# Kernel optimization log

Hardware: AMD Instinct MI355X
Metric: run time of the kernel (lower is better)

## Reference

```python
import jax, jax.numpy as jnp
import numpy as np


def _ln(x, g, b):
    m = x.mean(-1, keepdims=True)
    v = ((x - m) ** 2).mean(-1, keepdims=True)
    return (x - m) * jax.lax.rsqrt(v + 1e-5) * g + b


def _forward(x, fx_in, pre_w1, pre_b1, pre_w2, pre_b2, placeholder,
             ln1_g, ln1_b, px_w, px_b, pfx_w, pfx_b, slice_w, slice_b, temp,
             q_w, k_w, v_w, out_w, out_b, ln2_g, ln2_b,
             mlp_w1, mlp_b1, mlp_w2, mlp_b2,
             ln3_g, ln3_b, head_w1, head_b1, head_w2, head_b2):
    # All linear weights are stored as [in, out] (pre-transposed vs torch nn.Linear).
    B, N, _ = x.shape
    L, H = temp.shape
    dh = slice_w.shape[1]
    gelu = lambda t: jax.nn.gelu(t, approximate=False)
    # preprocess MLP (n_layers=0, res=False): Linear -> GELU -> Linear
    h = jnp.concatenate([x, fx_in], axis=-1)
    h = gelu(h @ pre_w1 + pre_b1) @ pre_w2 + pre_b2
    h = h + placeholder  # learned [D] offset
    scale = 1.0 / jnp.sqrt(jnp.asarray(dh, h.dtype))
    for i in range(L):  # loop over structurally distinct layers
        y = _ln(h, ln1_g[i], ln1_b[i])
        # project to per-head features: bhnd
        fx_mid = (y @ pfx_w[i] + pfx_b[i]).reshape(B, N, H, dh).transpose(0, 2, 1, 3)
        x_mid = (y @ px_w[i] + px_b[i]).reshape(B, N, H, dh).transpose(0, 2, 1, 3)
        # soft slice assignment over G slices
        logits = jnp.einsum('bhnd,dg->bhng', x_mid, slice_w[i]) + slice_b[i]
        sw = jax.nn.softmax(logits / temp[i][None, :, None, None], axis=-1)  # bhng
        norm = sw.sum(axis=2)  # bhg
        tok = jnp.einsum('bhnd,bhng->bhgd', fx_mid, sw) / (norm + 1e-5)[..., None]
        # attention over G=slice_num tokens
        q = tok @ q_w[i]
        k = tok @ k_w[i]
        v = tok @ v_w[i]
        attn = jax.nn.softmax(jnp.einsum('bhgd,bhmd->bhgm', q, k) * scale, axis=-1)
        out_slice = jnp.einsum('bhgm,bhmd->bhgd', attn, v)
        # deslice back to points
        out_x = jnp.einsum('bhgd,bhng->bhnd', out_slice, sw)
        out_x = out_x.transpose(0, 2, 1, 3).reshape(B, N, H * dh)
        h = h + (out_x @ out_w[i] + out_b[i])
        z = _ln(h, ln2_g[i], ln2_b[i])
        h = h + (gelu(z @ mlp_w1[i] + mlp_b1[i]) @ mlp_w2[i] + mlp_b2[i])
    z = _ln(h, ln3_g, ln3_b)
    return gelu(z @ head_w1 + head_b1) @ head_w2 + head_b2


def setup_inputs() -> dict:
    key = jax.random.key(0)
    B, N, D, H, dh, G, L = 2, 16384, 256, 8, 32, 64, 5
    SP, FUN, OUT = 2, 4, 4
    ID = H * dh  # inner_dim == n_hidden
    MR = D * 1   # mlp_ratio=1
    ks = iter(jax.random.split(key, 64))
    nrm = lambda shape, s=0.02: jax.random.normal(next(ks), shape, jnp.float32) * s
    return dict(
        x=jax.random.normal(next(ks), (B, N, SP), jnp.float32),
        fx_in=jax.random.normal(next(ks), (B, N, FUN), jnp.float32),
        pre_w1=nrm((SP + FUN, 2 * D)), pre_b1=jnp.zeros((2 * D,), jnp.float32),
        pre_w2=nrm((2 * D, D)), pre_b2=jnp.zeros((D,), jnp.float32),
        placeholder=nrm((D,)),
        ln1_g=jnp.ones((L, D), jnp.float32), ln1_b=jnp.zeros((L, D), jnp.float32),
        px_w=nrm((L, D, ID)), px_b=jnp.zeros((L, ID), jnp.float32),
        pfx_w=nrm((L, D, ID)), pfx_b=jnp.zeros((L, ID), jnp.float32),
        slice_w=nrm((L, dh, G), 0.1), slice_b=jnp.zeros((L, G), jnp.float32),
        temp=0.5 * jnp.ones((L, H), jnp.float32),
        q_w=nrm((L, dh, dh), 0.1), k_w=nrm((L, dh, dh), 0.1), v_w=nrm((L, dh, dh), 0.1),
        out_w=nrm((L, ID, D)), out_b=jnp.zeros((L, D), jnp.float32),
        ln2_g=jnp.ones((L, D), jnp.float32), ln2_b=jnp.zeros((L, D), jnp.float32),
        mlp_w1=nrm((L, D, MR)), mlp_b1=jnp.zeros((L, MR), jnp.float32),
        mlp_w2=nrm((L, MR, D)), mlp_b2=jnp.zeros((L, D), jnp.float32),
        ln3_g=jnp.ones((D,), jnp.float32), ln3_b=jnp.zeros((D,), jnp.float32),
        head_w1=nrm((D, D)), head_b1=jnp.zeros((D,), jnp.float32),
        head_w2=nrm((D, OUT)), head_b2=jnp.zeros((OUT,), jnp.float32),
    )


def reference(x, fx_in, pre_w1, pre_b1, pre_w2, pre_b2, placeholder,
              ln1_g, ln1_b, px_w, px_b, pfx_w, pfx_b, slice_w, slice_b, temp,
              q_w, k_w, v_w, out_w, out_b, ln2_g, ln2_b,
              mlp_w1, mlp_b1, mlp_w2, mlp_b2,
              ln3_g, ln3_b, head_w1, head_b1, head_w2, head_b2):
    return _forward(x, fx_in, pre_w1, pre_b1, pre_w2, pre_b2, placeholder,
                    ln1_g, ln1_b, px_w, px_b, pfx_w, pfx_b, slice_w, slice_b, temp,
                    q_w, k_w, v_w, out_w, out_b, ln2_g, ln2_b,
                    mlp_w1, mlp_b1, mlp_w2, mlp_b2,
                    ln3_g, ln3_b, head_w1, head_b1, head_w2, head_b2)
```

## Files before the change

kernel.cpp:

```cpp
#include <hip/hip_runtime.h>


#define MTOK 32768
#define NB   16384

typedef unsigned short u16;
using short8 = __attribute__((ext_vector_type(8))) short;
using f4     = __attribute__((ext_vector_type(4))) float;

__device__ __forceinline__ float bfu(u16 u) {
    return __uint_as_float(((unsigned)u) << 16);
}
__device__ __forceinline__ u16 f2bf(float f) {
    unsigned u = __float_as_uint(f);
    u += 0x7FFFu + ((u >> 16) & 1u);
    return (u16)(u >> 16);
}
__device__ __forceinline__ float ldf(const void* p, int i, int isbf) {
    return isbf ? bfu(((const u16*)p)[i]) : ((const float*)p)[i];
}
__device__ __forceinline__ float4 dec4(ushort4 u) {
    return make_float4(bfu(u.x), bfu(u.y), bfu(u.z), bfu(u.w));
}
__device__ __forceinline__ float gelu_f(float x) {
    return 0.5f * x * (1.0f + erff(x * 0.7071067811865475f));
}

typedef __attribute__((address_space(1))) const unsigned int* as1p;
typedef __attribute__((address_space(3))) unsigned int* as3p;
__device__ __forceinline__ void gload_lds16(const u16* g, u16* l) {
    __builtin_amdgcn_global_load_lds((as1p)g, (as3p)l, 16, 0, 0);
}

#define F_H      ((size_t)0)
#define F_OS     ((size_t)8388608)
#define F_TOKP   ((size_t)8421376)
#define F_NORMP  ((size_t)10518528)
#define F_TOK    ((size_t)10584064)
#define F_NORM   ((size_t)10616832)
#define F_BIAS   ((size_t)10617856)
#define F_PARAMS ((size_t)10626048)
#define F_BF     ((size_t)10858884)
#define B_PB2C 0
#define B_OUTB 256
#define B_M1B  1536
#define B_M2B  2816
#define B_HB1  4096
#define B_SP   4352
#define B_END  8192
#define U_WT     ((size_t)0)
#define WT_PRE2  0
#define WT_HEAD1 131072
#define WT_SPFX  196608
#define WT_OUT   1179648
#define WT_MLP1  1507328
#define WT_MLP2  1835008
#define WT_END   2162688
#define U_Y   ((size_t)2162688)
#define U_XM  ((size_t)10551296)
#define U_FM  ((size_t)18939904)
#define U_SW  ((size_t)27328512)

#define P_X    0
#define P_FX   65536
#define P_W1   196608
#define P_B1   199680
#define P_LN1G 200192
#define P_LN1B 201472
#define P_LN2G 202752
#define P_LN2B 204032
#define P_LN3G 205312
#define P_LN3B 205568
#define P_SLW  205824
#define P_SLB  216064
#define P_TEMP 216384
#define P_QW   216448
#define P_KW   221568
#define P_VW   226688
#define P_HW2  231808
#define P_HB2  232832
#define P_END  232836

__global__ __launch_bounds__(256) void cvt_kernel(
    const void* x, const void* fx, const void* w1, const void* b1,
    const void* l1g, const void* l1b, const void* l2g, const void* l2b,
    const void* l3g, const void* l3b, const void* slw, const void* slb,
    const void* tmp, const void* qw, const void* kw, const void* vw,
    const void* hw2, const void* hb2, float* __restrict__ P)
{
    int isbf = (((const u16*)tmp)[0] != 0);
    int idx = blockIdx.x * 256 + threadIdx.x;
    const void* s; int o;
    if      (idx < 65536)  { s = x;   o = idx; }
    else if (idx < 196608) { s = fx;  o = idx - 65536; }
    else if (idx < 199680) { s = w1;  o = idx - 196608; }
    else if (idx < 200192) { s = b1;  o = idx - 199680; }
    else if (idx < 201472) { s = l1g; o = idx - 200192; }
    else if (idx < 202752) { s = l1b; o = idx - 201472; }
    else if (idx < 204032) { s = l2g; o = idx - 202752; }
    else if (idx < 205312) { s = l2b; o = idx - 204032; }
    else if (idx < 205568) { s = l3g; o = idx - 205312; }
    else if (idx < 205824) { s = l3b; o = idx - 205568; }
    else if (idx < 216064) { s = slw; o = idx - 205824; }
    else if (idx < 216384) { s = slb; o = idx - 216064; }
    else if (idx < 216424) { s = tmp; o = idx - 216384; }
    else if (idx < 216448) { return; }
    else if (idx < 221568) { s = qw;  o = idx - 216448; }
    else if (idx < 226688) { s = kw;  o = idx - 221568; }
    else if (idx < 231808) { s = vw;  o = idx - 226688; }
    else if (idx < 232832) { s = hw2; o = idx - 231808; }
    else if (idx < 232836) { s = hb2; o = idx - 232832; }
    else return;
    P[idx] = ldf(s, o, isbf);
}

__global__ __launch_bounds__(256) void prep_main(
    const void* pre_w2, const void* head_w1, const void* pfx_w,
    const void* out_w, const void* mlp_w1, const void* mlp_w2,
    const void* pre_b2, const void* placeholder, const void* pfx_b,
    const void* out_b, const void* mlp_b1, const void* mlp_b2,
    const void* head_b1, const void* tmp,
    u16* __restrict__ WT, float* __restrict__ BIAS)
{
    int isbf = (((const u16*)tmp)[0] != 0);
    int blk = blockIdx.x;
    int t = threadIdx.x;
    if (blk < 368) {
        __shared__ float tile[64][65];
        const void* src; size_t srcoff; size_t dbase; int dstride;
        int k0, n0;
        if (blk < 32) {
            int tk = blk >> 2, tn = blk & 3;
            src = pre_w2; srcoff = 0;
            k0 = tk * 64; n0 = tn * 64;
            dbase = WT_PRE2; dstride = 512;
        } else {
            int m = (blk - 32) >> 4, tl = (blk - 32) & 15;
            int tk = tl >> 2, tn = tl & 3;
            k0 = tk * 64; n0 = tn * 64; dstride = 256;
            if (m == 0)       { src = head_w1; srcoff = 0;               dbase = WT_HEAD1; }
            else if (m <= 5)  { int i = m - 1;  src = pfx_w;  srcoff = (size_t)i * 65536;
                                dbase = WT_SPFX + (size_t)i * 196608 + (size_t)512 * 256; }
            else if (m <= 10) { int i = m - 6;  src = out_w;  srcoff = (size_t)i * 65536;
                                dbase = WT_OUT + (size_t)i * 65536; }
            else if (m <= 15) { int i = m - 11; src = mlp_w1; srcoff = (size_t)i * 65536;
                                dbase = WT_MLP1 + (size_t)i * 65536; }
            else              { int i = m - 16; src = mlp_w2; srcoff = (size_t)i * 65536;
                                dbase = WT_MLP2 + (size_t)i * 65536; }
        }
#pragma unroll
        for (int p = 0; p < 16; ++p) {
            int flat = t + 256 * p;
            int r = flat >> 6, c = flat & 63;
            tile[r][c] = ldf(src, srcoff + (size_t)(k0 + r) * 256 + n0 + c, isbf);
        }
        __syncthreads();
#pragma unroll
        for (int p = 0; p < 16; ++p) {
            int flat = t + 256 * p;
            int r = flat >> 6, c = flat & 63;
            WT[dbase + (size_t)(n0 + r) * dstride + k0 + c] = f2bf(tile[c][r]);
        }
    } else {
        int idx = (blk - 368) * 256 + t;
        if (idx < 256) {
            BIAS[B_PB2C + idx] = ldf(pre_b2, idx, isbf) + ldf(placeholder, idx, isbf);
        } else if (idx < 1536) {
            int o = idx - 256;  BIAS[B_OUTB + o] = ldf(out_b, o, isbf);
        } else if (idx < 2816) {
            int o = idx - 1536; BIAS[B_M1B + o] = ldf(mlp_b1, o, isbf);
        } else if (idx < 4096) {
            int o = idx - 2816; BIAS[B_M2B + o] = ldf(mlp_b2, o, isbf);
        } else if (idx < 4352) {
            int o = idx - 4096; BIAS[B_HB1 + o] = ldf(head_b1, o, isbf);
        } else if (idx < 5632) {
            int o = idx - 4352;
            int i = o >> 8, c = o & 255;
            BIAS[B_SP + i * 768 + 512 + c] = ldf(pfx_b, o, isbf);
        }
    }
}

__global__ __launch_bounds__(256) void prep_pxsl(
    const void* px_w, const void* px_b, const void* slw, const void* slb,
    const void* tmp, u16* __restrict__ WT, float* __restrict__ BIAS)
{
    int isbf = (((const u16*)tmp)[0] != 0);
    __shared__ float pxs[64 * 33];
    __shared__ float sls[2048];
    int blk = blockIdx.x;
    int i = blk >> 5, h = (blk >> 2) & 7, kb = blk & 3;
    int t = threadIdx.x;
#pragma unroll
    for (int p = 0; p < 8; ++p) {
        int flat = t + 256 * p;
        sls[flat] = ldf(slw, i * 2048 + flat, isbf);
        int k = flat >> 5, d = flat & 31;
        pxs[k * 33 + d] = ldf(px_w, i * 65536 + (kb * 64 + k) * 256 + h * 32 + d, isbf);
    }
    __syncthreads();
    int k = t & 63, gb = t >> 6;
    float acc[16];
#pragma unroll
    for (int gi = 0; gi < 16; ++gi) acc[gi] = 0.f;
#pragma unroll
    for (int d = 0; d < 32; ++d) {
        float pv = pxs[k * 33 + d];
        const float* sp = sls + d * 64 + gb * 16;
#pragma unroll
        for (int gi = 0; gi < 16; ++gi) acc[gi] = fmaf(pv, sp[gi], acc[gi]);
    }
    u16* WTp = WT + WT_SPFX + (size_t)i * 196608;
#pragma unroll
    for (int gi = 0; gi < 16; ++gi) {
        int n = h * 64 + gb * 16 + gi;
        WTp[n * 256 + kb * 64 + k] = f2bf(acc[gi]);
    }
    if (kb == 0 && t < 64) {
        int g = t;
        float a = ldf(slb, i * 64 + g, isbf);
#pragma unroll
        for (int d = 0; d < 32; ++d)
            a = fmaf(ldf(px_b, i * 256 + h * 32 + d, isbf), sls[d * 64 + g], a);
        BIAS[B_SP + i * 768 + h * 64 + g] = a;
    }
}

__global__ __launch_bounds__(256) void pre1_kernel(
    const float* __restrict__ P, u16* __restrict__ HID)
{
    __shared__ float w1s[3072];
    __shared__ float b1s[512];
    int t = threadIdx.x;
#pragma unroll
    for (int p = 0; p < 12; ++p) w1s[t + 256 * p] = P[P_W1 + t + 256 * p];
    b1s[t] = P[P_B1 + t];
    b1s[t + 256] = P[P_B1 + t + 256];
    __syncthreads();
    int m = blockIdx.x * 4 + (t >> 6);
    int lane = t & 63;
    float xa = P[P_X + m * 2],      xb = P[P_X + m * 2 + 1];
    float fa = P[P_FX + m * 4],     fb = P[P_FX + m * 4 + 1];
    float fc = P[P_FX + m * 4 + 2], fd = P[P_FX + m * 4 + 3];
    size_t base = (size_t)m * 512 + lane;
#pragma unroll
    for (int jj = 0; jj < 8; ++jj) {
        int j = lane + 64 * jj;
        float a = b1s[j];
        a = fmaf(xa, w1s[j], a);
        a = fmaf(xb, w1s[512 + j], a);
        a = fmaf(fa, w1s[1024 + j], a);
        a = fmaf(fb, w1s[1536 + j], a);
        a = fmaf(fc, w1s[2048 + j], a);
        a = fmaf(fd, w1s[2560 + j], a);
        HID[base + 64 * jj] = f2bf(gelu_f(a));
    }
}

template <int KK, bool RES>
__global__ __launch_bounds__(256, 3) void gemm_ln(
    const u16* __restrict__ A, const u16* __restrict__ Wt,
    const float* __restrict__ bias, const float* __restrict__ lng,
    const float* __restrict__ lnb, u16* __restrict__ Hb, u16* __restrict__ Y)
{
    __shared__ u16 As[64 * 64];
    __shared__ u16 Bs[256 * 64];
    __shared__ float rs2[2][64], rq2[2][64];
    const int t = threadIdx.x;
    const int wave = t >> 6, lane = t & 63;
    const int quad = lane >> 4, l15 = lane & 15;
    const int m0 = blockIdx.x * 64;
    const int wm = (wave & 1) * 32, wn = (wave >> 1) * 128;
    const int lrow = lane >> 3, ls = lane & 7;
    f4 acc[2][8];
#pragma unroll
    for (int i = 0; i < 2; ++i)
#pragma unroll
        for (int j = 0; j < 8; ++j) acc[i][j] = (f4){0.f, 0.f, 0.f, 0.f};

    for (int kc = 0; kc < KK; kc += 64) {
        if (kc) __syncthreads();
#pragma unroll
        for (int q = 0; q < 10; ++q) {
            int gr = wave * 80 + q * 8;
            if (gr < 64) {
                int row = gr + lrow;
                int chunk = ls ^ lrow;
                gload_lds16(A + (size_t)(m0 + row) * KK + kc + chunk * 8,
                            As + gr * 64);
            } else {
                int brow = gr - 64 + lrow;
                int chunk = ls ^ lrow;
                gload_lds16(Wt + (size_t)brow * KK + kc + chunk * 8,
                            Bs + (gr - 64) * 64);
            }
        }
        __syncthreads();
#pragma unroll
        for (int kk = 0; kk < 2; ++kk) {
            short8 a[2], b[8];
#pragma unroll
            for (int i = 0; i < 2; ++i) {
                int R = wm + i * 16 + l15;
                a[i] = *(const short8*)(As + R * 64 + (((quad + kk * 4) ^ (R & 7)) << 3));
            }
#pragma unroll
            for (int j = 0; j < 8; ++j) {
                int Rb = wn + j * 16 + l15;
                b[j] = *(const short8*)(Bs + Rb * 64 + (((quad + kk * 4) ^ (Rb & 7)) << 3));
            }
#pragma unroll
            for (int i = 0; i < 2; ++i)
#pragma unroll
                for (int j = 0; j < 8; ++j)
                    acc[i][j] = __builtin_amdgcn_mfma_f32_16x16x32_bf16(
                        a[i], b[j], acc[i][j], 0, 0, 0);
        }
    }
    int colj[8];
    float bj[8];
#pragma unroll
    for (int j = 0; j < 8; ++j) { colj[j] = wn + j * 16 + l15; bj[j] = bias[colj[j]]; }
    const int half = wn >> 7;
#pragma unroll
    for (int i = 0; i < 2; ++i) {
#pragma unroll
        for (int r = 0; r < 4; ++r) {
            int row = wm + i * 16 + quad * 4 + r;
            size_t gbase = (size_t)(m0 + row) * 256;
            float s = 0.f, q2 = 0.f;
#pragma unroll
            for (int j = 0; j < 8; ++j) {
                float v = acc[i][j][r] + bj[j];
                if (RES) v += bfu(Hb[gbase + colj[j]]);
                Hb[gbase + colj[j]] = f2bf(v);
                acc[i][j][r] = v;
                s += v; q2 += v * v;
            }
#pragma unroll
            for (int o = 1; o < 16; o <<= 1) { s += __shfl_xor(s, o); q2 += __shfl_xor(q2, o); }
            if (l15 == 0) { rs2[half][row] = s; rq2[half][row] = q2; }
        }
    }
    __syncthreads();
    float gj[8], betj[8];
#pragma unroll
    for (int j = 0; j < 8; ++j) { gj[j] = lng[colj[j]]; betj[j] = lnb[colj[j]]; }
#pragma unroll
    for (int i = 0; i < 2; ++i) {
#pragma unroll
        for (int r = 0; r < 4; ++r) {
            int row = wm + i * 16 + quad * 4 + r;
            size_t gbase = (size_t)(m0 + row) * 256;
            float mean = (rs2[0][row] + rs2[1][row]) * (1.0f / 256.0f);
            float var = (rq2[0][row] + rq2[1][row]) * (1.0f / 256.0f) - mean * mean;
            float rstd = rsqrtf(var + 1e-5f);
#pragma unroll
            for (int j = 0; j < 8; ++j) {
                float y = (acc[i][j][r] - mean) * rstd * gj[j] + betj[j];
                Y[gbase + colj[j]] = f2bf(y);
            }
        }
    }
}

__global__ __launch_bounds__(256, 4) void gemm_gelu(
    const u16* __restrict__ A, const u16* __restrict__ Wt,
    const float* __restrict__ bias, u16* __restrict__ Cb)
{
    __shared__ u16 As[128 * 64];
    __shared__ u16 Bs[128 * 64];
    const int t = threadIdx.x;
    const int wave = t >> 6, lane = t & 63;
    const int quad = lane >> 4, l15 = lane & 15;
    const int m0 = blockIdx.x * 128;
    const int n0 = blockIdx.y * 128;
    const int wm = (wave & 1) * 64, wn = (wave >> 1) * 64;
    const int r0 = wave * 32;
    const int lrow = lane >> 3, ls = lane & 7;
    f4 acc[4][4];
#pragma unroll
    for (int i = 0; i < 4; ++i)
#pragma unroll
        for (int j = 0; j < 4; ++j) acc[i][j] = (f4){0.f, 0.f, 0.f, 0.f};

    for (int kc = 0; kc < 256; kc += 64) {
        if (kc) __syncthreads();
#pragma unroll
        for (int q = 0; q < 4; ++q) {
            int row = r0 + q * 8 + lrow;
            int chunk = ls ^ (row & 7);
            gload_lds16(A  + (size_t)(m0 + row) * 256 + kc + chunk * 8,
                        As + (r0 + q * 8) * 64);
            gload_lds16(Wt + (size_t)(n0 + row) * 256 + kc + chunk * 8,
                        Bs + (r0 + q * 8) * 64);
        }
        __syncthreads();
#pragma unroll
        for (int kk = 0; kk < 2; ++kk) {
            short8 a[4], b[4];
#pragma unroll
            for (int i = 0; i < 4; ++i) {
                int R = wm + i * 16 + l15;
                a[i] = *(const short8*)(As + R * 64 + (((quad + kk * 4) ^ (R & 7)) << 3));
            }
#pragma unroll
            for (int j = 0; j < 4; ++j) {
                int R = wn + j * 16 + l15;
                b[j] = *(const short8*)(Bs + R * 64 + (((quad + kk * 4) ^ (R & 7)) << 3));
            }
#pragma unroll
            for (int i = 0; i < 4; ++i)
#pragma unroll
                for (int j = 0; j < 4; ++j)
                    acc[i][j] = __builtin_amdgcn_mfma_f32_16x16x32_bf16(
                        a[i], b[j], acc[i][j], 0, 0, 0);
        }
    }
#pragma unroll
    for (int j = 0; j < 4; ++j) {
        int cj = n0 + wn + j * 16 + l15;
        float bj = bias[cj];
#pragma unroll
        for (int i = 0; i < 4; ++i) {
            int rbase = m0 + wm + i * 16 + quad * 4;
#pragma unroll
            for (int r = 0; r < 4; ++r) {
                float v = gelu_f(acc[i][j][r] + bj);
                Cb[(size_t)(rbase + r) * 256 + cj] = f2bf(v);
            }
        }
    }
}

__global__ __launch_bounds__(256, 4) void gemm_spfx(
    const u16* __restrict__ A, const u16* __restrict__ Wt,
    const float* __restrict__ bsp, const float* __restrict__ tempv,
    u16* __restrict__ SW, u16* __restrict__ FM)
{
    __shared__ u16 As[128 * 64];
    __shared__ u16 Bs[128 * 64];
    const int t = threadIdx.x;
    const int wave = t >> 6, lane = t & 63;
    const int quad = lane >> 4, l15 = lane & 15;
    const int m0 = blockIdx.x * 128;
    const int n0 = blockIdx.y * 128;
    const int wm = (wave & 1) * 64, wn = (wave >> 1) * 64;
    const int r0 = wave * 32;
    const int lrow = lane >> 3, ls = lane & 7;
    f4 acc[4][4];
#pragma unroll
    for (int i = 0; i < 4; ++i)
#pragma unroll
        for (int j = 0; j < 4; ++j) acc[i][j] = (f4){0.f, 0.f, 0.f, 0.f};

    for (int kc = 0; kc < 256; kc += 64) {
        if (kc) __syncthreads();
#pragma unroll
        for (int q = 0; q < 4; ++q) {
            int row = r0 + q * 8 + lrow;
            int chunk = ls ^ (row & 7);
            gload_lds16(A  + (size_t)(m0 + row) * 256 + kc + chunk * 8,
                        As + (r0 + q * 8) * 64);
            gload_lds16(Wt + (size_t)(n0 + row) * 256 + kc + chunk * 8,
                        Bs + (r0 + q * 8) * 64);
        }
        __syncthreads();
#pragma unroll
        for (int kk = 0; kk < 2; ++kk) {
            short8 a[4], b[4];
#pragma unroll
            for (int i = 0; i < 4; ++i) {
                int R = wm + i * 16 + l15;
                a[i] = *(const short8*)(As + R * 64 + (((quad + kk * 4) ^ (R & 7)) << 3));
            }
#pragma unroll
            for (int j = 0; j < 4; ++j) {
                int R = wn + j * 16 + l15;
                b[j] = *(const short8*)(Bs + R * 64 + (((quad + kk * 4) ^ (R & 7)) << 3));
            }
#pragma unroll
            for (int i = 0; i < 4; ++i)
#pragma unroll
                for (int j = 0; j < 4; ++j)
                    acc[i][j] = __builtin_amdgcn_mfma_f32_16x16x32_bf16(
                        a[i], b[j], acc[i][j], 0, 0, 0);
        }
    }
    float bj[4];
#pragma unroll
    for (int j = 0; j < 4; ++j) bj[j] = bsp[n0 + wn + j * 16 + l15];
    if (blockIdx.y < 4) {
        const int h = (n0 + wn) >> 6;
        const float itemp = 1.0f / tempv[h];
#pragma unroll
        for (int i = 0; i < 4; ++i) {
#pragma unroll
            for (int r = 0; r < 4; ++r) {
                float v[4];
                float mx = -3.0e38f;
#pragma unroll
                for (int j = 0; j < 4; ++j) {
                    v[j] = (acc[i][j][r] + bj[j]) * itemp;
                    mx = fmaxf(mx, v[j]);
                }
#pragma unroll
                for (int o = 1; o < 16; o <<= 1) mx = fmaxf(mx, __shfl_xor(mx, o));
                float s = 0.f;
#pragma unroll
                for (int j = 0; j < 4; ++j) { v[j] = expf(v[j] - mx); s += v[j]; }
#pragma unroll
                for (int o = 1; o < 16; o <<= 1) s += __shfl_xor(s, o);
                float inv = 1.0f / s;
                int m = m0 + wm + i * 16 + quad * 4 + r;
                int b = m >> 14, n = m & 16383;
                size_t base = (((size_t)(b * 8 + h)) * NB + n) * 64;
#pragma unroll
                for (int j = 0; j < 4; ++j)
                    SW[base + j * 16 + l15] = f2bf(v[j] * inv);
            }
        }
    } else {
        int cj = (n0 - 512) + wn + l15;
#pragma unroll
        for (int j = 0; j < 4; ++j) {
            int col = cj + j * 16;
#pragma unroll
            for (int i = 0; i < 4; ++i) {
                int rbase = m0 + wm + i * 16 + quad * 4;
#pragma unroll
                for (int r = 0; r < 4; ++r)
                    FM[(size_t)(rbase + r) * 256 + col] = f2bf(acc[i][j][r] + bj[j]);
            }
        }
    }
}

__global__ __launch_bounds__(256) void tok1_kernel(
    const u16* __restrict__ FM, const u16* __restrict__ SW,
    float* __restrict__ TOKP, float* __restrict__ NORMP)
{
    int bh = blockIdx.x >> 6, chunk = blockIdx.x & 63;
    int b = bh >> 3, hd = bh & 7;
    int t = threadIdx.x, wave = t >> 6, lane = t & 63;
    int g0 = (lane >> 3) * 8, d0 = (lane & 7) * 4;
    float4 acc[8];
#pragma unroll
    for (int gi = 0; gi < 8; ++gi) acc[gi] = make_float4(0.f, 0.f, 0.f, 0.f);
    float4 n0a = make_float4(0.f, 0.f, 0.f, 0.f);
    float4 n1a = make_float4(0.f, 0.f, 0.f, 0.f);
    int nbase = chunk * 256 + wave * 64;
    const u16* fmB = FM + ((size_t)b * NB + nbase) * 256 + hd * 32 + d0;
    const u16* swB = SW + ((size_t)bh * NB + nbase) * 64 + g0;
    for (int j = 0; j < 64; ++j) {
        float4 f4v = dec4(*(const ushort4*)(fmB + (size_t)j * 256));
        float4 s0 = dec4(*(const ushort4*)(swB + (size_t)j * 64));
        float4 s1 = dec4(*(const ushort4*)(swB + (size_t)j * 64 + 4));
#define TOKACC(gi, sv)                                            \
        acc[gi].x = fmaf(f4v.x, sv, acc[gi].x);                   \
        acc[gi].y = fmaf(f4v.y, sv, acc[gi].y);                   \
        acc[gi].z = fmaf(f4v.z, sv, acc[gi].z);                   \
        acc[gi].w = fmaf(f4v.w, sv, acc[gi].w);
        TOKACC(0, s0.x) TOKACC(1, s0.y) TOKACC(2, s0.z) TOKACC(3, s0.w)
        TOKACC(4, s1.x) TOKACC(5, s1.y) TOKACC(6, s1.z) TOKACC(7, s1.w)
#undef TOKACC
        n0a.x += s0.x; n0a.y += s0.y; n0a.z += s0.z; n0a.w += s0.w;
        n1a.x += s1.x; n1a.y += s1.y; n1a.z += s1.z; n1a.w += s1.w;
    }
    __shared__ float red[4][2048];
    __shared__ float nred[4][64];
#pragma unroll
    for (int gi = 0; gi < 8; ++gi)
        *(float4*)&red[wave][(g0 + gi) * 32 + d0] = acc[gi];
    if ((lane & 7) == 0) {
        nred[wave][g0 + 0] = n0a.x; nred[wave][g0 + 1] = n0a.y;
        nred[wave][g0 + 2] = n0a.z; nred[wave][g0 + 3] = n0a.w;
        nred[wave][g0 + 4] = n1a.x; nred[wave][g0 + 5] = n1a.y;
        nred[wave][g0 + 6] = n1a.z; nred[wave][g0 + 7] = n1a.w;
    }
    __syncthreads();
    size_t tokBase = (size_t)(chunk * 16 + bh) * 2048;
#pragma unroll
    for (int k = 0; k < 8; ++k) {
        int c = t + 256 * k;
        TOKP[tokBase + c] = red[0][c] + red[1][c] + red[2][c] + red[3][c];
    }
    if (t < 64)
        NORMP[(chunk * 16 + bh) * 64 + t] = nred[0][t] + nred[1][t] + nred[2][t] + nred[3][t];
}

__global__ __launch_bounds__(256) void tok2_kernel(
    const float* __restrict__ TOKP, const float* __restrict__ NORMP,
    float* __restrict__ TOK, float* __restrict__ NORM)
{
    int idx = blockIdx.x * 256 + threadIdx.x;
    if (idx < 32768) {
        int bh = idx >> 11, c = idx & 2047;
        float s = 0.f;
#pragma unroll 8
        for (int ch = 0; ch < 64; ++ch) s += TOKP[(size_t)(ch * 16 + bh) * 2048 + c];
        TOK[idx] = s;
    } else if (idx < 33792) {
        int o = idx - 32768;
        int bh = o >> 6, g = o & 63;
        float s = 0.f;
#pragma unroll 8
        for (int ch = 0; ch < 64; ++ch) s += NORMP[(ch * 16 + bh) * 64 + g];
        NORM[o] = s;
    }
}

__global__ __launch_bounds__(256) void attn_kernel(
    const float* __restrict__ TOK, const float* __restrict__ NORM,
    const float* __restrict__ qw, const float* __restrict__ kw,
    const float* __restrict__ vw, float* __restrict__ OS)
{
    __shared__ float tokd[2048], qs[2048], ks[2048], vs[2048];
    int bh = blockIdx.x;
    int t = threadIdx.x;
#pragma unroll
    for (int i = 0; i < 2; ++i) {
        int f4v = t + 256 * i;
        float4 v = *(const float4*)(TOK + (size_t)bh * 2048 + f4v * 4);
        float inv = 1.0f / (NORM[bh * 64 + (f4v >> 3)] + 1e-5f);
        v.x *= inv; v.y *= inv; v.z *= inv; v.w *= inv;
        *(float4*)&tokd[f4v * 4] = v;
    }
    __syncthreads();
#pragma unroll
    for (int i = 0; i < 8; ++i) {
        int f = t + 256 * i;
        int g = f >> 5, d = f & 31;
        const float* tr = tokd + g * 32;
        float aq = 0.f, ak = 0.f, av = 0.f;
#pragma unroll
        for (int e = 0; e < 32; ++e) {
            float tv = tr[e];
            aq = fmaf(tv, qw[e * 32 + d], aq);
            ak = fmaf(tv, kw[e * 32 + d], ak);
            av = fmaf(tv, vw[e * 32 + d], av);
        }
        qs[f] = aq; ks[f] = ak; vs[f] = av;
    }
    __syncthreads();
    int g = t >> 2, sub = t & 3;
    float4 qv[8];
#pragma unroll
    for (int e4 = 0; e4 < 8; ++e4) qv[e4] = *(const float4*)(qs + g * 32 + e4 * 4);
    float p[16];
    float mx = -3.0e38f;
#pragma unroll
    for (int mm = 0; mm < 16; ++mm) {
        int mI = sub * 16 + mm;
        const float4* kr = (const float4*)(ks + mI * 32);
        float s = 0.f;
#pragma unroll
        for (int e4 = 0; e4 < 8; ++e4) {
            float4 kv = kr[e4];
            s = fmaf(qv[e4].x, kv.x, s); s = fmaf(qv[e4].y, kv.y, s);
            s = fmaf(qv[e4].z, kv.z, s); s = fmaf(qv[e4].w, kv.w, s);
        }
        s *= 0.17677669529663687f;
        p[mm] = s;
        mx = fmaxf(mx, s);
    }
    mx = fmaxf(mx, __shfl_xor(mx, 1));
    mx = fmaxf(mx, __shfl_xor(mx, 2));
    float lsum = 0.f;
#pragma unroll
    for (int mm = 0; mm < 16; ++mm) { p[mm] = expf(p[mm] - mx); lsum += p[mm]; }
    lsum += __shfl_xor(lsum, 1);
    lsum += __shfl_xor(lsum, 2);
    float inv = 1.0f / lsum;
    float4 oa[8];
#pragma unroll
    for (int d4 = 0; d4 < 8; ++d4) oa[d4] = make_float4(0.f, 0.f, 0.f, 0.f);
#pragma unroll
    for (int mm = 0; mm < 16; ++mm) {
        int mI = sub * 16 + mm;
        const float4* vr = (const float4*)(vs + mI * 32);
        float pm = p[mm];
#pragma unroll
        for (int d4 = 0; d4 < 8; ++d4) {
            float4 vv = vr[d4];
            oa[d4].x = fmaf(pm, vv.x, oa[d4].x);
            oa[d4].y = fmaf(pm, vv.y, oa[d4].y);
            oa[d4].z = fmaf(pm, vv.z, oa[d4].z);
            oa[d4].w = fmaf(pm, vv.w, oa[d4].w);
        }
    }
#pragma unroll
    for (int d4 = 0; d4 < 8; ++d4) {
        oa[d4].x += __shfl_xor(oa[d4].x, 1); oa[d4].x += __shfl_xor(oa[d4].x, 2);
        oa[d4].y += __shfl_xor(oa[d4].y, 1); oa[d4].y += __shfl_xor(oa[d4].y, 2);
        oa[d4].z += __shfl_xor(oa[d4].z, 1); oa[d4].z += __shfl_xor(oa[d4].z, 2);
        oa[d4].w += __shfl_xor(oa[d4].w, 1); oa[d4].w += __shfl_xor(oa[d4].w, 2);
    }
    float4 r0 = oa[sub * 2], r1 = oa[sub * 2 + 1];
    r0.x *= inv; r0.y *= inv; r0.z *= inv; r0.w *= inv;
    r1.x *= inv; r1.y *= inv; r1.z *= inv; r1.w *= inv;
    *(float4*)(OS + (size_t)bh * 2048 + g * 32 + sub * 8)     = r0;
    *(float4*)(OS + (size_t)bh * 2048 + g * 32 + sub * 8 + 4) = r1;
}

__global__ __launch_bounds__(256) void deslice_kernel(
    const float* __restrict__ OS, const u16* __restrict__ SW, u16* __restrict__ OX)
{
    __shared__ float swt[8 * 16 * 64];
    int blk = blockIdx.x;
    int b = blk >> 10, n0 = (blk & 1023) * 16;
    int t = threadIdx.x;
    int hd = t >> 5, d = t & 31;
#pragma unroll
    for (int i = 0; i < 8; ++i) {
        int f4v = t + 256 * i;
        int hd2 = f4v >> 8, mm = (f4v >> 4) & 15, g4 = f4v & 15;
        ushort4 u = *(const ushort4*)(SW + (((size_t)(b * 8 + hd2)) * NB + n0 + mm) * 64 + g4 * 4);
        *(float4*)&swt[(hd2 * 16 + mm) * 64 + g4 * 4] = dec4(u);
    }
    __syncthreads();
    float acc[16];
#pragma unroll
    for (int mm = 0; mm < 16; ++mm) acc[mm] = 0.f;
    const float* osb = OS + ((size_t)(b * 8 + hd)) * 2048 + d;
#pragma unroll 4
    for (int g4 = 0; g4 < 16; ++g4) {
        float o0 = osb[(g4 * 4 + 0) * 32], o1 = osb[(g4 * 4 + 1) * 32];
        float o2 = osb[(g4 * 4 + 2) * 32], o3 = osb[(g4 * 4 + 3) * 32];
        const float* swp = swt + hd * 1024 + g4 * 4;
#pragma unroll
        for (int mm = 0; mm < 16; ++mm) {
            float4 sv = *(const float4*)(swp + mm * 64);
            acc[mm] = fmaf(o0, sv.x, fmaf(o1, sv.y, fmaf(o2, sv.z, fmaf(o3, sv.w, acc[mm]))));
        }
    }
#pragma unroll
    for (int mm = 0; mm < 16; ++mm)
        OX[((size_t)b * NB + n0 + mm) * 256 + t] = f2bf(acc[mm]);
}

__global__ __launch_bounds__(256) void head2_kernel(
    const u16* __restrict__ HID, const float* __restrict__ w2,
    const float* __restrict__ b2, const void* tmp, void* __restrict__ OUT)
{
    int isbf = (((const u16*)tmp)[0] != 0);
    int lane = threadIdx.x & 63;
    size_t m = (size_t)blockIdx.x * 4 + (threadIdx.x >> 6);
    const float4 hv = dec4(*(const ushort4*)(HID + m * 256 + lane * 4));
    float4 a = make_float4(0.f, 0.f, 0.f, 0.f);
    float hcomp[4] = {hv.x, hv.y, hv.z, hv.w};
#pragma unroll
    for (int i = 0; i < 4; ++i) {
        const float4 wv = *(const float4*)(w2 + (lane * 4 + i) * 4);
        float h = hcomp[i];
        a.x = fmaf(h, wv.x, a.x); a.y = fmaf(h, wv.y, a.y);
        a.z = fmaf(h, wv.z, a.z); a.w = fmaf(h, wv.w, a.w);
    }
#pragma unroll
    for (int o = 32; o; o >>= 1) {
        a.x += __shfl_xor(a.x, o); a.y += __shfl_xor(a.y, o);
        a.z += __shfl_xor(a.z, o); a.w += __shfl_xor(a.w, o);
    }
    if (lane == 0) {
        float o0 = a.x + b2[0], o1 = a.y + b2[1], o2 = a.z + b2[2], o3 = a.w + b2[3];
        if (isbf) {
            ushort4 r; r.x = f2bf(o0); r.y = f2bf(o1); r.z = f2bf(o2); r.w = f2bf(o3);
            *(ushort4*)((u16*)OUT + m * 4) = r;
        } else {
            *(float4*)((float*)OUT + m * 4) = make_float4(o0, o1, o2, o3);
        }
    }
}

extern "C" void kernel_launch(void* const* d_in, const int* in_sizes, int n_in,
                              void* d_out, int out_size, void* d_ws, size_t ws_size,
                              hipStream_t stream)
{
    const void* x = d_in[0];      const void* fx = d_in[1];
    const void* pre_w1 = d_in[2]; const void* pre_b1 = d_in[3];
    const void* pre_w2 = d_in[4]; const void* pre_b2 = d_in[5];
    const void* placeholder = d_in[6];
    const void* ln1_g = d_in[7];  const void* ln1_b = d_in[8];
    const void* px_w = d_in[9];   const void* px_b = d_in[10];
    const void* pfx_w = d_in[11]; const void* pfx_b = d_in[12];
    const void* slice_w = d_in[13]; const void* slice_b = d_in[14];
    const void* temp = d_in[15];
    const void* q_w = d_in[16];   const void* k_w = d_in[17]; const void* v_w = d_in[18];
    const void* out_w = d_in[19]; const void* out_b = d_in[20];
    const void* ln2_g = d_in[21]; const void* ln2_b = d_in[22];
    const void* mlp_w1 = d_in[23]; const void* mlp_b1 = d_in[24];
    const void* mlp_w2 = d_in[25]; const void* mlp_b2 = d_in[26];
    const void* ln3_g = d_in[27]; const void* ln3_b = d_in[28];
    const void* head_w1 = d_in[29]; const void* head_b1 = d_in[30];
    const void* head_w2 = d_in[31]; const void* head_b2 = d_in[32];

    float* ws = (float*)d_ws;
    u16*   Hb    = (u16*)(ws + F_H);
    float* OSp   = ws + F_OS;
    float* TOKP  = ws + F_TOKP;
    float* NORMP = ws + F_NORMP;
    float* TOKf  = ws + F_TOK;
    float* NORMf = ws + F_NORM;
    float* BIAS  = ws + F_BIAS;
    float* P     = ws + F_PARAMS;
    u16*   U     = (u16*)(ws + F_BF);
    u16*   WT    = U + U_WT;
    u16*   Yb    = U + U_Y;
    u16*   XMb   = U + U_XM;
    u16*   FMb   = U + U_FM;
    u16*   SWb   = U + U_SW;
    u16*   HIDb  = U + U_XM;

    cvt_kernel<<<910, 256, 0, stream>>>(x, fx, pre_w1, pre_b1, ln1_g, ln1_b,
        ln2_g, ln2_b, ln3_g, ln3_b, slice_w, slice_b, temp, q_w, k_w, v_w,
        head_w2, head_b2, P);
    prep_main<<<390, 256, 0, stream>>>(pre_w2, head_w1, pfx_w, out_w, mlp_w1,
        mlp_w2, pre_b2, placeholder, pfx_b, out_b, mlp_b1, mlp_b2, head_b1,
        temp, WT, BIAS);
    prep_pxsl<<<160, 256, 0, stream>>>(px_w, px_b, slice_w, slice_b, temp, WT, BIAS);
    pre1_kernel<<<8192, 256, 0, stream>>>(P, HIDb);

    dim3 gpl(256, 2);
    dim3 gsp(256, 6);
    gemm_ln<512, false><<<512, 256, 0, stream>>>(HIDb, WT + WT_PRE2,
        BIAS + B_PB2C, P + P_LN1G, P + P_LN1B, Hb, Yb);

    for (int i = 0; i < 5; ++i) {
        gemm_spfx<<<gsp, 256, 0, stream>>>(Yb, WT + WT_SPFX + (size_t)i * 196608,
            BIAS + B_SP + i * 768, P + P_TEMP + i * 8, SWb, FMb);
        tok1_kernel<<<1024, 256, 0, stream>>>(FMb, SWb, TOKP, NORMP);
        tok2_kernel<<<132, 256, 0, stream>>>(TOKP, NORMP, TOKf, NORMf);
        attn_kernel<<<16, 256, 0, stream>>>(TOKf, NORMf, P + P_QW + i * 1024,
            P + P_KW + i * 1024, P + P_VW + i * 1024, OSp);
        deslice_kernel<<<2048, 256, 0, stream>>>(OSp, SWb, Yb);
        gemm_ln<256, true><<<512, 256, 0, stream>>>(Yb, WT + WT_OUT + i * 65536,
            BIAS + B_OUTB + i * 256, P + P_LN2G + i * 256, P + P_LN2B + i * 256, Hb, Yb);
        gemm_gelu<<<gpl, 256, 0, stream>>>(Yb, WT + WT_MLP1 + i * 65536,
            BIAS + B_M1B + i * 256, XMb);
        const float* ng = (i < 4) ? (P + P_LN1G + (i + 1) * 256) : (P + P_LN3G);
        const float* nb = (i < 4) ? (P + P_LN1B + (i + 1) * 256) : (P + P_LN3B);
        gemm_ln<256, true><<<512, 256, 0, stream>>>(XMb, WT + WT_MLP2 + i * 65536,
            BIAS + B_M2B + i * 256, ng, nb, Hb, Yb);
    }

    gemm_gelu<<<gpl, 256, 0, stream>>>(Yb, WT + WT_HEAD1, BIAS + B_HB1, XMb);
    head2_kernel<<<8192, 256, 0, stream>>>(XMb, P + P_HW2, P + P_HB2, temp, d_out);
}
```

Before: 1.113 ms.

## Load GEMM MFMA operands directly from global memory instead of LDS staging

The three GEMM kernels (gemm_ln, gemm_gelu, gemm_spfx) no longer stage A and W tiles through shared memory with global_load_lds and barriers. Each lane now reads its short8 MFMA fragments straight from global memory into registers, and the k-loop is unrolled by two. This removes the LDS traffic, the __syncthreads barriers and the LDS footprint, which may allow more occupancy. The cost is no data sharing between waves, so each weight fragment is fetched repeatedly from L2/global with strided 16-byte accesses, and there is no software pipelining to hide load latency.

After: 1.359 ms. +22.1%, slower.

```diff
diff --git a/kernel.cpp b/kernel.cpp
--- a/kernel.cpp
+++ b/kernel.cpp
@@ -24,12 +24,6 @@
 }
 __device__ __forceinline__ float gelu_f(float x) {
     return 0.5f * x * (1.0f + erff(x * 0.7071067811865475f));
-}
-
-typedef __attribute__((address_space(1))) const unsigned int* as1p;
-typedef __attribute__((address_space(3))) unsigned int* as3p;
-__device__ __forceinline__ void gload_lds16(const u16* g, u16* l) {
-    __builtin_amdgcn_global_load_lds((as1p)g, (as3p)l, 16, 0, 0);
 }
 
 #define F_H      ((size_t)0)
@@ -263,59 +257,35 @@
     const float* __restrict__ bias, const float* __restrict__ lng,
     const float* __restrict__ lnb, u16* __restrict__ Hb, u16* __restrict__ Y)
 {
-    __shared__ u16 As[64 * 64];
-    __shared__ u16 Bs[256 * 64];
     __shared__ float rs2[2][64], rq2[2][64];
     const int t = threadIdx.x;
     const int wave = t >> 6, lane = t & 63;
     const int quad = lane >> 4, l15 = lane & 15;
     const int m0 = blockIdx.x * 64;
     const int wm = (wave & 1) * 32, wn = (wave >> 1) * 128;
-    const int lrow = lane >> 3, ls = lane & 7;
     f4 acc[2][8];
 #pragma unroll
     for (int i = 0; i < 2; ++i)
 #pragma unroll
         for (int j = 0; j < 8; ++j) acc[i][j] = (f4){0.f, 0.f, 0.f, 0.f};
 
-    for (int kc = 0; kc < KK; kc += 64) {
-        if (kc) __syncthreads();
-#pragma unroll
-        for (int q = 0; q < 10; ++q) {
-            int gr = wave * 80 + q * 8;
-            if (gr < 64) {
-                int row = gr + lrow;
-                int chunk = ls ^ lrow;
-                gload_lds16(A + (size_t)(m0 + row) * KK + kc + chunk * 8,
-                            As + gr * 64);
-            } else {
-                int brow = gr - 64 + lrow;
-                int chunk = ls ^ lrow;
-                gload_lds16(Wt + (size_t)brow * KK + kc + chunk * 8,
-                            Bs + (gr - 64) * 64);
-            }
-        }
-        __syncthreads();
-#pragma unroll
-        for (int kk = 0; kk < 2; ++kk) {
-            short8 a[2], b[8];
-#pragma unroll
-            for (int i = 0; i < 2; ++i) {
-                int R = wm + i * 16 + l15;
-                a[i] = *(const short8*)(As + R * 64 + (((quad + kk * 4) ^ (R & 7)) << 3));
-            }
-#pragma unroll
-            for (int j = 0; j < 8; ++j) {
-                int Rb = wn + j * 16 + l15;
-                b[j] = *(const short8*)(Bs + Rb * 64 + (((quad + kk * 4) ^ (Rb & 7)) << 3));
-            }
-#pragma unroll
-            for (int i = 0; i < 2; ++i)
-#pragma unroll
-                for (int j = 0; j < 8; ++j)
-                    acc[i][j] = __builtin_amdgcn_mfma_f32_16x16x32_bf16(
-                        a[i], b[j], acc[i][j], 0, 0, 0);
-        }
+    const u16* Ab = A  + (size_t)(m0 + wm + l15) * KK + quad * 8;
+    const u16* Bb = Wt + (size_t)(wn + l15) * KK + quad * 8;
+#pragma unroll 2
+    for (int kk = 0; kk < KK / 32; ++kk) {
+        short8 a[2], b[8];
+#pragma unroll
+        for (int i = 0; i < 2; ++i)
+            a[i] = *(const short8*)(Ab + (size_t)i * 16 * KK + kk * 32);
+#pragma unroll
+        for (int j = 0; j < 8; ++j)
+            b[j] = *(const short8*)(Bb + (size_t)j * 16 * KK + kk * 32);
+#pragma unroll
+        for (int i = 0; i < 2; ++i)
+#pragma unroll
+            for (int j = 0; j < 8; ++j)
+                acc[i][j] = __builtin_amdgcn_mfma_f32_16x16x32_bf16(
+                    a[i], b[j], acc[i][j], 0, 0, 0);
     }
     int colj[8];
     float bj[8];
@@ -368,54 +338,34 @@
     const u16* __restrict__ A, const u16* __restrict__ Wt,
     const float* __restrict__ bias, u16* __restrict__ Cb)
 {
-    __shared__ u16 As[128 * 64];
-    __shared__ u16 Bs[128 * 64];
     const int t = threadIdx.x;
     const int wave = t >> 6, lane = t & 63;
     const int quad = lane >> 4, l15 = lane & 15;
     const int m0 = blockIdx.x * 128;
     const int n0 = blockIdx.y * 128;
     const int wm = (wave & 1) * 64, wn = (wave >> 1) * 64;
-    const int r0 = wave * 32;
-    const int lrow = lane >> 3, ls = lane & 7;
     f4 acc[4][4];
 #pragma unroll
     for (int i = 0; i < 4; ++i)
 #pragma unroll
         for (int j = 0; j < 4; ++j) acc[i][j] = (f4){0.f, 0.f, 0.f, 0.f};
 
-    for (int kc = 0; kc < 256; kc += 64) {
-        if (kc) __syncthreads();
-#pragma unroll
-        for (int q = 0; q < 4; ++q) {
-            int row = r0 + q * 8 + lrow;
-            int chunk = ls ^ (row & 7);
-            gload_lds16(A  + (size_t)(m0 + row) * 256 + kc + chunk * 8,
-                        As + (r0 + q * 8) * 64);
-            gload_lds16(Wt + (size_t)(n0 + row) * 256 + kc + chunk * 8,
-                        Bs + (r0 + q * 8) * 64);
-        }
-        __syncthreads();
-#pragma unroll
-        for (int kk = 0; kk < 2; ++kk) {
-            short8 a[4], b[4];
-#pragma unroll
-            for (int i = 0; i < 4; ++i) {
-                int R = wm + i * 16 + l15;
-                a[i] = *(const short8*)(As + R * 64 + (((quad + kk * 4) ^ (R & 7)) << 3));
-            }
-#pragma unroll
-            for (int j = 0; j < 4; ++j) {
-                int R = wn + j * 16 + l15;
-                b[j] = *(const short8*)(Bs + R * 64 + (((quad + kk * 4) ^ (R & 7)) << 3));
-            }
-#pragma unroll
-            for (int i = 0; i < 4; ++i)
-#pragma unroll
-                for (int j = 0; j < 4; ++j)
-                    acc[i][j] = __builtin_amdgcn_mfma_f32_16x16x32_bf16(
-                        a[i], b[j], acc[i][j], 0, 0, 0);
-        }
+    const u16* Ab = A  + (size_t)(m0 + wm + l15) * 256 + quad * 8;
+    const u16* Bb = Wt + (size_t)(n0 + wn + l15) * 256 + quad * 8;
+#pragma unroll 2
+    for (int kk = 0; kk < 8; ++kk) {
+        short8 a[4], b[4];
+#pragma unroll
+        for (int i = 0; i < 4; ++i) {
+            a[i] = *(const short8*)(Ab + (size_t)i * 16 * 256 + kk * 32);
+            b[i] = *(const short8*)(Bb + (size_t)i * 16 * 256 + kk * 32);
+        }
+#pragma unroll
+        for (int i = 0; i < 4; ++i)
+#pragma unroll
+            for (int j = 0; j < 4; ++j)
+                acc[i][j] = __builtin_amdgcn_mfma_f32_16x16x32_bf16(
+                    a[i], b[j], acc[i][j], 0, 0, 0);
     }
 #pragma unroll
     for (int j = 0; j < 4; ++j) {
@@ -438,54 +388,34 @@
     const float* __restrict__ bsp, const float* __restrict__ tempv,
     u16* __restrict__ SW, u16* __restrict__ FM)
 {
-    __shared__ u16 As[128 * 64];
-    __shared__ u16 Bs[128 * 64];
     const int t = threadIdx.x;
     const int wave = t >> 6, lane = t & 63;
     const int quad = lane >> 4, l15 = lane & 15;
     const int m0 = blockIdx.x * 128;
     const int n0 = blockIdx.y * 128;
     const int wm = (wave & 1) * 64, wn = (wave >> 1) * 64;
-    const int r0 = wave * 32;
-    const int lrow = lane >> 3, ls = lane & 7;
     f4 acc[4][4];
 #pragma unroll
     for (int i = 0; i < 4; ++i)
 #pragma unroll
         for (int j = 0; j < 4; ++j) acc[i][j] = (f4){0.f, 0.f, 0.f, 0.f};
 
-    for (int kc = 0; kc < 256; kc += 64) {
-        if (kc) __syncthreads();
-#pragma unroll
-        for (int q = 0; q < 4; ++q) {
-            int row = r0 + q * 8 + lrow;
-            int chunk = ls ^ (row & 7);
-            gload_lds16(A  + (size_t)(m0 + row) * 256 + kc + chunk * 8,
-                        As + (r0 + q * 8) * 64);
-            gload_lds16(Wt + (size_t)(n0 + row) * 256 + kc + chunk * 8,
-                        Bs + (r0 + q * 8) * 64);
-        }
-        __syncthreads();
-#pragma unroll
-        for (int kk = 0; kk < 2; ++kk) {
-            short8 a[4], b[4];
-#pragma unroll
-            for (int i = 0; i < 4; ++i) {
-                int R = wm + i * 16 + l15;
-                a[i] = *(const short8*)(As + R * 64 + (((quad + kk * 4) ^ (R & 7)) << 3));
-            }
-#pragma unroll
-            for (int j = 0; j < 4; ++j) {
-                int R = wn + j * 16 + l15;
-                b[j] = *(const short8*)(Bs + R * 64 + (((quad + kk * 4) ^ (R & 7)) << 3));
-            }
-#pragma unroll
-            for (int i = 0; i < 4; ++i)
-#pragma unroll
-                for (int j = 0; j < 4; ++j)
-                    acc[i][j] = __builtin_amdgcn_mfma_f32_16x16x32_bf16(
-                        a[i], b[j], acc[i][j], 0, 0, 0);
-        }
+    const u16* Ab = A  + (size_t)(m0 + wm + l15) * 256 + quad * 8;
+    const u16* Bb = Wt + (size_t)(n0 + wn + l15) * 256 + quad * 8;
+#pragma unroll 2
+    for (int kk = 0; kk < 8; ++kk) {
+        short8 a[4], b[4];
+#pragma unroll
+        for (int i = 0; i < 4; ++i) {
+            a[i] = *(const short8*)(Ab + (size_t)i * 16 * 256 + kk * 32);
+            b[i] = *(const short8*)(Bb + (size_t)i * 16 * 256 + kk * 32);
+        }
+#pragma unroll
+        for (int i = 0; i < 4; ++i)
+#pragma unroll
+            for (int j = 0; j < 4; ++j)
+                acc[i][j] = __builtin_amdgcn_mfma_f32_16x16x32_bf16(
+                    a[i], b[j], acc[i][j], 0, 0, 0);
     }
     float bj[4];
 #pragma unroll
```

## Fuse MLP up-projection, GELU and down-projection into one kernel

Applied to the files above, without the earlier changes.

Replaces the separate gemm_gelu and gemm_ln launches for the per-layer MLP with a single kernel. Each block computes a 64-row tile of the hidden activation, keeps the GELU output in shared memory, then multiplies it by W2 and applies the residual add and the next LayerNorm. This avoids writing the intermediate activation to global memory and reading it back, and saves one launch per layer. The cost is a larger shared-memory footprint (about 50KB), an occupancy bound of 2 blocks per CU, and 64-row tiles that reload the full weight matrices for every block.

Measured after the change: 1.047 ms (median of 2 runs). -5.8%, faster.

```diff
diff --git a/kernel.cpp b/kernel.cpp
--- a/kernel.cpp
+++ b/kernel.cpp
@@ -364,6 +364,163 @@
     }
 }
 
+__global__ __launch_bounds__(256, 2) void gemm_mlp(
+    const u16* __restrict__ A, const u16* __restrict__ W1,
+    const float* __restrict__ b1, const u16* __restrict__ W2,
+    const float* __restrict__ b2, const float* __restrict__ lng,
+    const float* __restrict__ lnb, u16* __restrict__ Hb, u16* __restrict__ Y)
+{
+    __shared__ u16 As[64 * 64];
+    __shared__ u16 Bs[256 * 64];
+    __shared__ u16 hs[64 * 264];
+    __shared__ float rs2[2][64], rq2[2][64];
+    const int t = threadIdx.x;
+    const int wave = t >> 6, lane = t & 63;
+    const int quad = lane >> 4, l15 = lane & 15;
+    const int m0 = blockIdx.x * 64;
+    const int wm = (wave & 1) * 32, wn = (wave >> 1) * 128;
+    const int lrow = lane >> 3, ls = lane & 7;
+    f4 acc[2][8];
+#pragma unroll
+    for (int i = 0; i < 2; ++i)
+#pragma unroll
+        for (int j = 0; j < 8; ++j) acc[i][j] = (f4){0.f, 0.f, 0.f, 0.f};
+
+    for (int kc = 0; kc < 256; kc += 64) {
+        if (kc) __syncthreads();
+#pragma unroll
+        for (int q = 0; q < 10; ++q) {
+            int gr = wave * 80 + q * 8;
+            if (gr < 64) {
+                int row = gr + lrow;
+                gload_lds16(A + (size_t)(m0 + row) * 256 + kc + (ls ^ lrow) * 8,
+                            As + gr * 64);
+            } else {
+                int brow = gr - 64 + lrow;
+                gload_lds16(W1 + (size_t)brow * 256 + kc + (ls ^ lrow) * 8,
+                            Bs + (gr - 64) * 64);
+            }
+        }
+        __syncthreads();
+#pragma unroll
+        for (int kk = 0; kk < 2; ++kk) {
+            short8 a[2], b[8];
+#pragma unroll
+            for (int i = 0; i < 2; ++i) {
+                int R = wm + i * 16 + l15;
+                a[i] = *(const short8*)(As + R * 64 + (((quad + kk * 4) ^ (R & 7)) << 3));
+            }
+#pragma unroll
+            for (int j = 0; j < 8; ++j) {
+                int Rb = wn + j * 16 + l15;
+                b[j] = *(const short8*)(Bs + Rb * 64 + (((quad + kk * 4) ^ (Rb & 7)) << 3));
+            }
+#pragma unroll
+            for (int i = 0; i < 2; ++i)
+#pragma unroll
+                for (int j = 0; j < 8; ++j)
+                    acc[i][j] = __builtin_amdgcn_mfma_f32_16x16x32_bf16(
+                        a[i], b[j], acc[i][j], 0, 0, 0);
+        }
+    }
+    int colj[8];
+#pragma unroll
+    for (int j = 0; j < 8; ++j) colj[j] = wn + j * 16 + l15;
+    {
+        float bj[8];
+#pragma unroll
+        for (int j = 0; j < 8; ++j) bj[j] = b1[colj[j]];
+#pragma unroll
+        for (int i = 0; i < 2; ++i)
+#pragma unroll
+            for (int r = 0; r < 4; ++r) {
+                int row = wm + i * 16 + quad * 4 + r;
+#pragma unroll
+                for (int j = 0; j < 8; ++j)
+                    hs[row * 264 + colj[j]] = f2bf(gelu_f(acc[i][j][r] + bj[j]));
+            }
+    }
+#pragma unroll
+    for (int i = 0; i < 2; ++i)
+#pragma unroll
+        for (int j = 0; j < 8; ++j) acc[i][j] = (f4){0.f, 0.f, 0.f, 0.f};
+
+    for (int kc = 0; kc < 256; kc += 64) {
+        __syncthreads();
+#pragma unroll
+        for (int q = 0; q < 8; ++q) {
+            int gr = wave * 64 + q * 8;
+            int brow = gr + lrow;
+            gload_lds16(W2 + (size_t)brow * 256 + kc + (ls ^ lrow) * 8,
+                        Bs + gr * 64);
+        }
+        __syncthreads();
+#pragma unroll
+        for (int kk = 0; kk < 2; ++kk) {
+            short8 a[2], b[8];
+#pragma unroll
+            for (int i = 0; i < 2; ++i) {
+                int R = wm + i * 16 + l15;
+                a[i] = *(const short8*)(hs + R * 264 + kc + kk * 32 + quad * 8);
+            }
+#pragma unroll
+            for (int j = 0; j < 8; ++j) {
+                int Rb = wn + j * 16 + l15;
+                b[j] = *(const short8*)(Bs + Rb * 64 + (((quad + kk * 4) ^ (Rb & 7)) << 3));
+            }
+#pragma unroll
+            for (int i = 0; i < 2; ++i)
+#pragma unroll
+                for (int j = 0; j < 8; ++j)
+                    acc[i][j] = __builtin_amdgcn_mfma_f32_16x16x32_bf16(
+                        a[i], b[j], acc[i][j], 0, 0, 0);
+        }
+    }
+    float bj[8];
+#pragma unroll
+    for (int j = 0; j < 8; ++j) bj[j] = b2[colj[j]];
+    const int half = wn >> 7;
+#pragma unroll
+    for (int i = 0; i < 2; ++i) {
+#pragma unroll
+        for (int r = 0; r < 4; ++r) {
+            int row = wm + i * 16 + quad * 4 + r;
+            size_t gbase = (size_t)(m0 + row) * 256;
+            float s = 0.f, q2 = 0.f;
+#pragma unroll
+            for (int j = 0; j < 8; ++j) {
+                float v = acc[i][j][r] + bj[j] + bfu(Hb[gbase + colj[j]]);
+                Hb[gbase + colj[j]] = f2bf(v);
+                acc[i][j][r] = v;
+                s += v; q2 += v * v;
+            }
+#pragma unroll
+            for (int o = 1; o < 16; o <<= 1) { s += __shfl_xor(s, o); q2 += __shfl_xor(q2, o); }
+            if (l15 == 0) { rs2[half][row] = s; rq2[half][row] = q2; }
+        }
+    }
+    __syncthreads();
+    float gj[8], betj[8];
+#pragma unroll
+    for (int j = 0; j < 8; ++j) { gj[j] = lng[colj[j]]; betj[j] = lnb[colj[j]]; }
+#pragma unroll
+    for (int i = 0; i < 2; ++i) {
+#pragma unroll
+        for (int r = 0; r < 4; ++r) {
+            int row = wm + i * 16 + quad * 4 + r;
+            size_t gbase = (size_t)(m0 + row) * 256;
+            float mean = (rs2[0][row] + rs2[1][row]) * (1.0f / 256.0f);
+            float var = (rq2[0][row] + rq2[1][row]) * (1.0f / 256.0f) - mean * mean;
+            float rstd = rsqrtf(var + 1e-5f);
+#pragma unroll
+            for (int j = 0; j < 8; ++j) {
+                float y = (acc[i][j][r] - mean) * rstd * gj[j] + betj[j];
+                Y[gbase + colj[j]] = f2bf(y);
+            }
+        }
+    }
+}
+
 __global__ __launch_bounds__(256, 4) void gemm_gelu(
     const u16* __restrict__ A, const u16* __restrict__ Wt,
     const float* __restrict__ bias, u16* __restrict__ Cb)
@@ -835,11 +992,10 @@
         deslice_kernel<<<2048, 256, 0, stream>>>(OSp, SWb, Yb);
         gemm_ln<256, true><<<512, 256, 0, stream>>>(Yb, WT + WT_OUT + i * 65536,
             BIAS + B_OUTB + i * 256, P + P_LN2G + i * 256, P + P_LN2B + i * 256, Hb, Yb);
-        gemm_gelu<<<gpl, 256, 0, stream>>>(Yb, WT + WT_MLP1 + i * 65536,
-            BIAS + B_M1B + i * 256, XMb);
         const float* ng = (i < 4) ? (P + P_LN1G + (i + 1) * 256) : (P + P_LN3G);
         const float* nb = (i < 4) ? (P + P_LN1B + (i + 1) * 256) : (P + P_LN3B);
-        gemm_ln<256, true><<<512, 256, 0, stream>>>(XMb, WT + WT_MLP2 + i * 65536,
+        gemm_mlp<<<512, 256, 0, stream>>>(Yb, WT + WT_MLP1 + i * 65536,
+            BIAS + B_M1B + i * 256, WT + WT_MLP2 + i * 65536,
             BIAS + B_M2B + i * 256, ng, nb, Hb, Yb);
     }
 
```
